# Kernel tuning notes

Measured on AMD Instinct MI355X. Metric: run time of the kernel, lower is better.

Reference implementation:

```python
import jax, jax.numpy as jnp
import numpy as np
import math

D_MODEL = 1024
N_HEADS = 16
D_K = D_MODEL // N_HEADS
BSZ = 4
SEQ = 2048


def setup_inputs() -> dict:
    key = jax.random.key(0)
    ks = jax.random.split(key, 10)
    x = jax.random.normal(ks[0], (BSZ, SEQ, D_MODEL), dtype=jnp.float32)
    pad_mask = jnp.zeros((BSZ, 1, 1, SEQ), dtype=jnp.int32)
    s = 0.02
    Wq = jax.random.normal(ks[1], (D_MODEL, D_MODEL), jnp.float32) * s
    bq = jax.random.normal(ks[2], (D_MODEL,), jnp.float32) * s
    Wk = jax.random.normal(ks[3], (D_MODEL, D_MODEL), jnp.float32) * s
    bk = jax.random.normal(ks[4], (D_MODEL,), jnp.float32) * s
    Wv = jax.random.normal(ks[5], (D_MODEL, D_MODEL), jnp.float32) * s
    bv = jax.random.normal(ks[6], (D_MODEL,), jnp.float32) * s
    Wo = jax.random.normal(ks[7], (D_MODEL, D_MODEL), jnp.float32) * s
    bo = jax.random.normal(ks[8], (D_MODEL,), jnp.float32) * s
    return {"x": x, "pad_mask": pad_mask, "Wq": Wq, "bq": bq, "Wk": Wk,
            "bk": bk, "Wv": Wv, "bv": bv, "Wo": Wo, "bo": bo}


def reference(x, pad_mask, Wq, bq, Wk, bk, Wv, bv, Wo, bo):
    bsz, seq_len, d_model = x.shape
    h, dk = N_HEADS, D_K

    def split(W, b):
        # torch Linear: x @ W.T + b ; then [b,s,h,dk] -> [b,h,s,dk]
        y = jnp.einsum('bsd,ed->bse', x, W) + b
        return y.reshape(bsz, seq_len, h, dk).transpose(0, 2, 1, 3)

    q = split(Wq, bq)
    k = split(Wk, bk)
    v = split(Wv, bv)

    scores = jnp.einsum('bhqd,bhkd->bhqk', q, k) / math.sqrt(dk)
    causal = jnp.triu(jnp.ones((seq_len, seq_len), dtype=bool), k=1)
    scores = jnp.where(causal[None, None], -jnp.inf, scores)
    scores = jnp.where(pad_mask == 1, -jnp.inf, scores)
    attn = jax.nn.softmax(scores, axis=-1)
    attn = jnp.nan_to_num(attn, nan=0.0)
    out = jnp.einsum('bhqk,bhkd->bhqd', attn, v)
    out = out.transpose(0, 2, 1, 3).reshape(bsz, seq_len, d_model)
    # dropout is identity in eval mode
    return jnp.einsum('bsd,ed->bse', out, Wo) + bo
```

## Files before the change

### kernel.cpp

```cpp
#include <hip/hip_runtime.h>
#include <stdint.h>
#include <stddef.h>


typedef __bf16 bf16;
typedef __bf16 bf16x8 __attribute__((ext_vector_type(8)));
typedef __bf16 bf16x4 __attribute__((ext_vector_type(4)));
typedef float f32x4 __attribute__((ext_vector_type(4)));

#define DM   1024
#define NH   16
#define DK   64
#define BSZ  4
#define SEQL 2048
#define NTOK 8192
#define NEGB -3.0e38f

__device__ __forceinline__ void async16(const bf16* g, void* l) {
  __builtin_amdgcn_global_load_lds(
      (__attribute__((address_space(1))) void*)g,
      (__attribute__((address_space(3))) void*)l, 16, 0, 0);
}

__global__ __launch_bounds__(256) void cvt_all(
    const float* __restrict__ x,
    const float* __restrict__ w0, const float* __restrict__ w1,
    const float* __restrict__ w2, const float* __restrict__ w3,
    const int* __restrict__ pad,
    bf16* __restrict__ xd,
    bf16* __restrict__ d0, bf16* __restrict__ d1,
    bf16* __restrict__ d2, bf16* __restrict__ d3,
    float* __restrict__ padf) {
  int blk = blockIdx.x;
  if (blk >= 6144) {
    int i = (blk - 6144) * 2048 + threadIdx.x * 8;
    int4 p0 = *(const int4*)(pad + i);
    int4 p1 = *(const int4*)(pad + i + 4);
    float4 o0 = {p0.x ? NEGB : 0.f, p0.y ? NEGB : 0.f, p0.z ? NEGB : 0.f, p0.w ? NEGB : 0.f};
    float4 o1 = {p1.x ? NEGB : 0.f, p1.y ? NEGB : 0.f, p1.z ? NEGB : 0.f, p1.w ? NEGB : 0.f};
    *(float4*)(padf + i) = o0;
    *(float4*)(padf + i + 4) = o1;
    return;
  }
  const float* s; bf16* d; int i;
  if (blk < 4096) { s = x; d = xd; i = blk * 2048 + threadIdx.x * 8; }
  else {
    int m = (blk - 4096) >> 9, bi = (blk - 4096) & 511;
    switch (m) {
      case 0:  s = w0; d = d0; break;
      case 1:  s = w1; d = d1; break;
      case 2:  s = w2; d = d2; break;
      default: s = w3; d = d3; break;
    }
    i = bi * 2048 + threadIdx.x * 8;
  }
  float4 v0 = *(const float4*)(s + i);
  float4 v1 = *(const float4*)(s + i + 4);
  bf16x8 o = {(bf16)v0.x, (bf16)v0.y, (bf16)v0.z, (bf16)v0.w,
              (bf16)v1.x, (bf16)v1.y, (bf16)v1.z, (bf16)v1.w};
  *(bf16x8*)(d + i) = o;
}

template <int OUT_MODE>
__device__ __forceinline__ void gemm_fine(const bf16* __restrict__ A,
                                          const bf16* __restrict__ W,
                                          const float* __restrict__ bias,
                                          void* __restrict__ outp,
                                          int bm, int bn, char* smem) {
  const int tid  = threadIdx.x;
  const int lane = tid & 63;
  const int wv   = tid >> 6;
  const int wr   = wv >> 2;
  const int wc   = wv & 3;
  const int c    = lane & 15;
  const int quad = lane >> 4;

  char* Ab = smem;
  char* Bb = smem + 24576;

  const int sr  = tid >> 2;
  const int sjj = ((tid & 3) ^ (sr & 3)) * 8;
  const bf16* gA = A + (size_t)(bm + sr) * DM + sjj;
  const bf16* gB = W + (size_t)(bn + sr) * DM + sjj;

#define STG(KT, U) {                                                     \
    async16(gA + (size_t)(KT) * 32, Ab + (U) * 8192 + tid * 16);         \
    async16(gB + (size_t)(KT) * 32, Bb + (U) * 16384 + tid * 16);        \
    async16(gB + (size_t)(KT) * 32 + (size_t)128 * DM,                   \
            Bb + (U) * 16384 + 8192 + tid * 16); }

  const int sw = (quad ^ (c & 3)) * 16;
  int aoff[4], boff[4];
#pragma unroll
  for (int i = 0; i < 4; ++i) {
    aoff[i] = (wr * 64 + i * 16 + c) * 64 + sw;
    boff[i] = (wc * 64 + i * 16 + c) * 64 + sw;
  }

  f32x4 acc[4][4] = {};

  STG(0, 0) STG(1, 1)
  asm volatile("s_waitcnt vmcnt(3)" ::: "memory");
  __builtin_amdgcn_s_barrier();
  __builtin_amdgcn_sched_barrier(0);

#pragma unroll
  for (int kt = 0; kt < 32; ++kt) {
    const char* Ac = Ab + (kt % 3) * 8192;
    const char* Bc = Bb + (kt % 3) * 16384;
    bf16x8 a[4], b[4];
#pragma unroll
    for (int i = 0; i < 4; ++i) a[i] = *(const bf16x8*)(Ac + aoff[i]);
#pragma unroll
    for (int i = 0; i < 4; ++i) b[i] = *(const bf16x8*)(Bc + boff[i]);
    if (kt + 2 < 32) STG(kt + 2, (kt + 2) % 3)
    __builtin_amdgcn_s_barrier();
    asm volatile("s_waitcnt lgkmcnt(0)" ::: "memory");
    __builtin_amdgcn_sched_barrier(0);
    __builtin_amdgcn_s_setprio(1);
#pragma unroll
    for (int mi = 0; mi < 4; ++mi)
#pragma unroll
      for (int ni = 0; ni < 4; ++ni)
        acc[mi][ni] = __builtin_amdgcn_mfma_f32_16x16x32_bf16(a[mi], b[ni],
                                                              acc[mi][ni], 0, 0, 0);
    __builtin_amdgcn_s_setprio(0);
    if (kt <= 29)      asm volatile("s_waitcnt vmcnt(3)" ::: "memory");
    else if (kt == 30) asm volatile("s_waitcnt vmcnt(0)" ::: "memory");
    if (kt != 31) {
      __builtin_amdgcn_s_barrier();
      __builtin_amdgcn_sched_barrier(0);
    }
  }
#undef STG

  float bias_r[4];
#pragma unroll
  for (int ni = 0; ni < 4; ++ni) bias_r[ni] = bias[bn + wc * 64 + ni * 16 + c];

  if constexpr (OUT_MODE == 2) {
    __syncthreads();
    bf16* vt = (bf16*)smem + wv * 4608;
#pragma unroll
    for (int mi = 0; mi < 4; ++mi)
#pragma unroll
      for (int ni = 0; ni < 4; ++ni) {
        bf16x4 pv = {(bf16)(acc[mi][ni][0] + bias_r[ni]),
                     (bf16)(acc[mi][ni][1] + bias_r[ni]),
                     (bf16)(acc[mi][ni][2] + bias_r[ni]),
                     (bf16)(acc[mi][ni][3] + bias_r[ni])};
        *(bf16x4*)&vt[(ni * 16 + c) * 72 + mi * 16 + quad * 4] = pv;
      }
    const int base = bm + wr * 64;
    const int bb = base >> 11, s0 = base & 2047;
    const int rl = lane >> 3, cl = lane & 7;
#pragma unroll
    for (int it = 0; it < 8; ++it) {
      int d_row = it * 8 + rl;
      bf16x8 v = *(const bf16x8*)&vt[d_row * 72 + cl * 8];
      int n_g = bn + wc * 64 + d_row;
      int hh = n_g >> 6, dd = n_g & 63;
      *(bf16x8*)&((bf16*)outp)[(((size_t)(bb * NH + hh)) * DK + dd) * SEQL + s0 + cl * 8] = v;
    }
    return;
  }

#pragma unroll
  for (int mi = 0; mi < 4; ++mi) {
#pragma unroll
    for (int reg = 0; reg < 4; ++reg) {
      int m_g = bm + wr * 64 + mi * 16 + quad * 4 + reg;
#pragma unroll
      for (int ni = 0; ni < 4; ++ni) {
        int n_g = bn + wc * 64 + ni * 16 + c;
        float v = acc[mi][ni][reg] + bias_r[ni];
        if constexpr (OUT_MODE == 0) {
          int b = m_g >> 11, s = m_g & 2047;
          int h = n_g >> 6, d = n_g & 63;
          ((bf16*)outp)[(((size_t)(b * NH + h) * SEQL + s) << 6) + d] = (bf16)v;
        } else {
          ((float*)outp)[(size_t)m_g * DM + n_g] = v;
        }
      }
    }
  }
}

__global__ __launch_bounds__(512, 4) void qkv_gemm(
    const bf16* __restrict__ X,
    const bf16* __restrict__ Wq, const bf16* __restrict__ Wk, const bf16* __restrict__ Wv,
    const float* __restrict__ bq, const float* __restrict__ bk, const float* __restrict__ bv,
    bf16* __restrict__ Q, bf16* __restrict__ K, bf16* __restrict__ Vt) {
  __shared__ alignas(16) char smem[73728];
  const int f   = blockIdx.x;
  const int xcd = f & 7;
  const int c96 = f >> 3;
  const int z   = c96 >> 5;
  const int r   = c96 & 31;
  const int bm  = (xcd * 8 + (r >> 2)) * 128;
  const int bn  = (r & 3) * 256;
  if (z == 0)      gemm_fine<0>(X, Wq, bq, Q,  bm, bn, smem);
  else if (z == 1) gemm_fine<0>(X, Wk, bk, K,  bm, bn, smem);
  else             gemm_fine<2>(X, Wv, bv, Vt, bm, bn, smem);
}

__global__ __launch_bounds__(512, 4) void out_gemm(const bf16* __restrict__ A,
                                                   const bf16* __restrict__ W,
                                                   const float* __restrict__ bias,
                                                   float* __restrict__ out) {
  __shared__ alignas(16) char smem[73728];
  const int f   = blockIdx.x;
  const int c32 = f >> 3;
  const int bm  = ((f & 7) * 8 + (c32 >> 2)) * 128;
  const int bn  = (c32 & 3) * 256;
  gemm_fine<1>(A, W, bias, out, bm, bn, smem);
}

__global__ __launch_bounds__(512, 2) void attn_kernel(
    const bf16* __restrict__ Q, const bf16* __restrict__ K,
    const bf16* __restrict__ Vt, const float* __restrict__ padf,
    bf16* __restrict__ O) {
  const int B = blockIdx.x;
  const int bh = (B & 7) + 8 * (B >> 5);
  const int t  = (B >> 3) & 3;
  const int b = bh >> 4, h = bh & 15;
  const int tid  = threadIdx.x;
  const int lane = tid & 63;
  const int wv   = tid >> 6;
  const int c    = lane & 15;
  const int quad = lane >> 4;

  __shared__ bf16 Ks[2][64 * 64];
  __shared__ bf16 Vs[2][64 * 64];
  __shared__ bf16 Pl_all[8][32 * 64];
  bf16* Pl = &Pl_all[wv][0];

  const bf16* Qh  = Q  + (size_t)bh * SEQL * DK;
  const bf16* Kh  = K  + (size_t)bh * SEQL * DK;
  const bf16* Vth = Vt + (size_t)bh * DK * SEQL;
  const float* pb = padf + b * SEQL;

  const int sr = tid >> 3;
  const int sj = ((tid & 7) ^ (sr & 7)) * 8;
  const bf16* gK = Kh  + (size_t)sr * DK   + sj;
  const bf16* gV = Vth + (size_t)sr * SEQL + sj;
  bf16* lK0 = &Ks[0][tid * 8]; bf16* lK1 = &Ks[1][tid * 8];
  bf16* lV0 = &Vs[0][tid * 8]; bf16* lV1 = &Vs[1][tid * 8];

  const float sc = 0.1803368801111204f;

  for (int pass = 0; pass < 2; ++pass) {
    const int qt  = pass ? 7 - t : t;
    const int R   = qt * 256 + wv * 32;
    const int nkt = (qt + 1) * 4;

    bf16x8 Qf[2][2];
#pragma unroll
    for (int qg = 0; qg < 2; ++qg)
#pragma unroll
      for (int kh = 0; kh < 2; ++kh)
        Qf[qg][kh] = *(const bf16x8*)&Qh[(size_t)(R + qg * 16 + c) * DK + kh * 32 + quad * 8];

    f32x4 Oc[2][4] = {};
    float ls[2] = {0.f, 0.f};

    __syncthreads();
    async16(gK, lK0);
    async16(gV, lV0);

    for (int kt = 0; kt < nkt; ++kt) {
      const int cur = kt & 1;
      const int kb = kt * 64;
      __syncthreads();

      if (kt + 1 < nkt) {
        async16(gK + (size_t)(kt + 1) * 64 * DK, cur ? lK0 : lK1);
        async16(gV + (size_t)(kt + 1) * 64,      cur ? lV0 : lV1);
      }
      if (kb > R + 31) continue;

      float4 bc[4];
#pragma unroll
      for (int kf = 0; kf < 4; ++kf)
        bc[kf] = *(const float4*)&pb[kb + kf * 16 + quad * 4];

      const bf16* Kc = cur ? Ks[1] : Ks[0];
      const bf16* Vc = cur ? Vs[1] : Vs[0];

      bf16x8 Kf[4][2], Vf[4][2];
#pragma unroll
      for (int kf = 0; kf < 4; ++kf)
#pragma unroll
        for (int kh = 0; kh < 2; ++kh)
          Kf[kf][kh] = *(const bf16x8*)&Kc[(kf * 16 + c) * 64 + (((kh * 4 + quad) ^ (c & 7)) * 8)];
#pragma unroll
      for (int df = 0; df < 4; ++df)
#pragma unroll
        for (int kv = 0; kv < 2; ++kv)
          Vf[df][kv] = *(const bf16x8*)&Vc[(df * 16 + c) * 64 + (((kv * 4 + quad) ^ (c & 7)) * 8)];

      f32x4 st[2][4] = {};
#pragma unroll
      for (int qg = 0; qg < 2; ++qg)
#pragma unroll
        for (int kh = 0; kh < 2; ++kh)
#pragma unroll
          for (int kf = 0; kf < 4; ++kf)
            st[qg][kf] = __builtin_amdgcn_mfma_f32_16x16x32_bf16(Kf[kf][kh], Qf[qg][kh],
                                                                 st[qg][kf], 0, 0, 0);

      if (kb + 63 > R) {
#pragma unroll
        for (int qg = 0; qg < 2; ++qg) {
          const int qrow = R + qg * 16 + c;
#pragma unroll
          for (int kf = 0; kf < 4; ++kf) {
            const float* bv4 = (const float*)&bc[kf];
            float p4[4];
#pragma unroll
            for (int r = 0; r < 4; ++r) {
              float e = __builtin_amdgcn_exp2f(__builtin_fmaf(st[qg][kf][r], sc, bv4[r]));
              if (kb + kf * 16 + quad * 4 + r > qrow) e = 0.f;
              p4[r] = e;
              ls[qg] += e;
            }
            bf16x4 pk = {(bf16)p4[0], (bf16)p4[1], (bf16)p4[2], (bf16)p4[3]};
            *(bf16x4*)&Pl[(qg * 16 + c) * 64 +
                          (((kf * 2 + (quad >> 1)) ^ (c & 7)) * 8) + (quad & 1) * 4] = pk;
          }
        }
      } else {
#pragma unroll
        for (int qg = 0; qg < 2; ++qg) {
#pragma unroll
          for (int kf = 0; kf < 4; ++kf) {
            const float* bv4 = (const float*)&bc[kf];
            float p4[4];
#pragma unroll
            for (int r = 0; r < 4; ++r) {
              float e = __builtin_amdgcn_exp2f(__builtin_fmaf(st[qg][kf][r], sc, bv4[r]));
              p4[r] = e;
              ls[qg] += e;
            }
            bf16x4 pk = {(bf16)p4[0], (bf16)p4[1], (bf16)p4[2], (bf16)p4[3]};
            *(bf16x4*)&Pl[(qg * 16 + c) * 64 +
                          (((kf * 2 + (quad >> 1)) ^ (c & 7)) * 8) + (quad & 1) * 4] = pk;
          }
        }
      }

#pragma unroll
      for (int qg = 0; qg < 2; ++qg)
#pragma unroll
        for (int kv = 0; kv < 2; ++kv) {
          bf16x8 af = *(const bf16x8*)&Pl[(qg * 16 + c) * 64 +
                                          (((kv * 4 + quad) ^ (c & 7)) * 8)];
#pragma unroll
          for (int df = 0; df < 4; ++df)
            Oc[qg][df] = __builtin_amdgcn_mfma_f32_16x16x32_bf16(af, Vf[df][kv],
                                                                 Oc[qg][df], 0, 0, 0);
        }
    }

#pragma unroll
    for (int qg = 0; qg < 2; ++qg) {
      float l = ls[qg];
      l += __shfl_xor(l, 16);
      l += __shfl_xor(l, 32);
      float linv = (l > 0.f) ? 1.f / l : 0.f;
      float lr[4];
#pragma unroll
      for (int r = 0; r < 4; ++r) lr[r] = __shfl(linv, quad * 4 + r);
#pragma unroll
      for (int r = 0; r < 4; ++r) {
        size_t row = (size_t)(b * SEQL + R + qg * 16 + quad * 4 + r) * DM + h * DK;
#pragma unroll
        for (int df = 0; df < 4; ++df)
          O[row + df * 16 + c] = (bf16)(Oc[qg][df][r] * lr[r]);
      }
    }
  }
}

extern "C" void kernel_launch(void* const* d_in, const int* in_sizes, int n_in,
                              void* d_out, int out_size, void* d_ws, size_t ws_size,
                              hipStream_t stream) {
  const float* x   = (const float*)d_in[0];
  const int*   pad = (const int*)d_in[1];
  const float* Wq  = (const float*)d_in[2];
  const float* bq  = (const float*)d_in[3];
  const float* Wk  = (const float*)d_in[4];
  const float* bk  = (const float*)d_in[5];
  const float* Wv  = (const float*)d_in[6];
  const float* bv  = (const float*)d_in[7];
  const float* Wo  = (const float*)d_in[8];
  const float* bo  = (const float*)d_in[9];
  float* out = (float*)d_out;

  const size_t SZ_X = (size_t)NTOK * DM * 2;
  const size_t SZ_W = (size_t)DM * DM * 2;
  char* ws = (char*)d_ws;
  bf16* Xb  = (bf16*)ws;  ws += SZ_X;
  bf16* Wqb = (bf16*)ws;  ws += SZ_W;
  bf16* Wkb = (bf16*)ws;  ws += SZ_W;
  bf16* Wvb = (bf16*)ws;  ws += SZ_W;
  bf16* Wob = (bf16*)ws;  ws += SZ_W;
  bf16* Qb  = (bf16*)ws;  ws += SZ_X;
  bf16* Kb  = (bf16*)ws;  ws += SZ_X;
  bf16* Vtb = (bf16*)ws;  ws += SZ_X;
  bf16* Ob  = (bf16*)ws;  ws += SZ_X;
  float* padfb = (float*)ws; ws += (size_t)NTOK * 4;

  cvt_all<<<6148, 256, 0, stream>>>(x, Wq, Wk, Wv, Wo, pad,
                                    Xb, Wqb, Wkb, Wvb, Wob, padfb);
  qkv_gemm<<<768, 512, 0, stream>>>(Xb, Wqb, Wkb, Wvb, bq, bk, bv, Qb, Kb, Vtb);
  attn_kernel<<<256, 512, 0, stream>>>(Qb, Kb, Vtb, padfb, Ob);
  out_gemm<<<256, 512, 0, stream>>>(Ob, Wob, bo, out);
}
```

Before: 237.1 us.

## Software-pipeline PV MFMA one tile behind QK in attention loop

Restructures the flash-attention inner loop so the P·V matrix multiply for the previous key tile is issued right after the current tile's Q·K multiply. V fragments are carried in registers across iterations, and a final epilogue drains the last tile. The goal is to overlap the softmax/exp work and LDS round-trip of P with MFMA execution. The cost is more register pressure, and correctness depends on the P buffer from the previous tile staying intact until it is read.

```diff
diff --git a/kernel.cpp b/kernel.cpp
--- a/kernel.cpp
+++ b/kernel.cpp
@@ -253,6 +253,7 @@
     const int qt  = pass ? 7 - t : t;
     const int R   = qt * 256 + wv * 32;
     const int nkt = (qt + 1) * 4;
+    const int lim = qt * 4 + (wv >> 1) + 1;
 
     bf16x8 Qf[2][2];
 #pragma unroll
@@ -263,6 +264,7 @@
 
     f32x4 Oc[2][4] = {};
     float ls[2] = {0.f, 0.f};
+    bf16x8 VfP[4][2];
 
     __syncthreads();
     async16(gK, lK0);
@@ -277,7 +279,7 @@
         async16(gK + (size_t)(kt + 1) * 64 * DK, cur ? lK0 : lK1);
         async16(gV + (size_t)(kt + 1) * 64,      cur ? lV0 : lV1);
       }
-      if (kb > R + 31) continue;
+      if (kt >= lim) continue;
 
       float4 bc[4];
 #pragma unroll
@@ -287,17 +289,22 @@
       const bf16* Kc = cur ? Ks[1] : Ks[0];
       const bf16* Vc = cur ? Vs[1] : Vs[0];
 
-      bf16x8 Kf[4][2], Vf[4][2];
+      bf16x8 Kf[4][2];
 #pragma unroll
       for (int kf = 0; kf < 4; ++kf)
 #pragma unroll
         for (int kh = 0; kh < 2; ++kh)
           Kf[kf][kh] = *(const bf16x8*)&Kc[(kf * 16 + c) * 64 + (((kh * 4 + quad) ^ (c & 7)) * 8)];
-#pragma unroll
-      for (int df = 0; df < 4; ++df)
-#pragma unroll
-        for (int kv = 0; kv < 2; ++kv)
-          Vf[df][kv] = *(const bf16x8*)&Vc[(df * 16 + c) * 64 + (((kv * 4 + quad) ^ (c & 7)) * 8)];
+
+      bf16x8 afr[2][2];
+      if (kt > 0) {
+#pragma unroll
+        for (int qg = 0; qg < 2; ++qg)
+#pragma unroll
+          for (int kv = 0; kv < 2; ++kv)
+            afr[qg][kv] = *(const bf16x8*)&Pl[(qg * 16 + c) * 64 +
+                                              (((kv * 4 + quad) ^ (c & 7)) * 8)];
+      }
 
       f32x4 st[2][4] = {};
 #pragma unroll
@@ -308,6 +315,23 @@
           for (int kf = 0; kf < 4; ++kf)
             st[qg][kf] = __builtin_amdgcn_mfma_f32_16x16x32_bf16(Kf[kf][kh], Qf[qg][kh],
                                                                  st[qg][kf], 0, 0, 0);
+
+      if (kt > 0) {
+#pragma unroll
+        for (int qg = 0; qg < 2; ++qg)
+#pragma unroll
+          for (int kv = 0; kv < 2; ++kv)
+#pragma unroll
+            for (int df = 0; df < 4; ++df)
+              Oc[qg][df] = __builtin_amdgcn_mfma_f32_16x16x32_bf16(afr[qg][kv], VfP[df][kv],
+                                                                   Oc[qg][df], 0, 0, 0);
+      }
+
+#pragma unroll
+      for (int df = 0; df < 4; ++df)
+#pragma unroll
+        for (int kv = 0; kv < 2; ++kv)
+          VfP[df][kv] = *(const bf16x8*)&Vc[(df * 16 + c) * 64 + (((kv * 4 + quad) ^ (c & 7)) * 8)];
 
       if (kb + 63 > R) {
 #pragma unroll
@@ -348,7 +372,9 @@
           }
         }
       }
-
+    }
+
+    {
 #pragma unroll
       for (int qg = 0; qg < 2; ++qg)
 #pragma unroll
@@ -357,7 +383,7 @@
                                           (((kv * 4 + quad) ^ (c & 7)) * 8)];
 #pragma unroll
           for (int df = 0; df < 4; ++df)
-            Oc[qg][df] = __builtin_amdgcn_mfma_f32_16x16x32_bf16(af, Vf[df][kv],
+            Oc[qg][df] = __builtin_amdgcn_mfma_f32_16x16x32_bf16(af, VfP[df][kv],
                                                                  Oc[qg][df], 0, 0, 0);
         }
     }
```

Result: no change. 233.1 us (-1.7%).
